# Performance work log

Hardware: AMD Instinct MI355X
Metric: run time of the kernel (lower is better)

## Reference

```python
import jax, jax.numpy as jnp
import numpy as np

N = 50000   # num_nodes
E = 640000  # num_edges (avg degree ~12.8)
D = 128     # input_dim
H = 128     # hidden_dim
T = 100     # targets per head


def setup_inputs() -> dict:
    key = jax.random.key(0)
    ks = jax.random.split(key, 20)
    w = lambda k, s: jax.random.normal(k, s, jnp.float32) * 0.02
    return {
        "x": jax.random.normal(ks[0], (N, D), jnp.float32),
        "edge_index": jax.random.randint(ks[1], (2, E), 0, N, dtype=jnp.int32),
        "edge_weight": jax.random.uniform(ks[2], (E,), jnp.float32),
        "ace_idx": jax.random.randint(ks[3], (T,), 0, N, dtype=jnp.int32),
        "h2_idx": jax.random.randint(ks[4], (T,), 0, N, dtype=jnp.int32),
        "W1": w(ks[5], (D, H)), "b1": jnp.zeros((H,), jnp.float32),
        "W2": w(ks[6], (H, H)), "b2": jnp.zeros((H,), jnp.float32),
        "W3": w(ks[7], (H, H)), "b3": jnp.zeros((H,), jnp.float32),
        "Wh": w(ks[8], (H, H)), "bh": jnp.zeros((H,), jnp.float32),
        "Wace": w(ks[9], (H, 1)), "bace": jnp.zeros((1,), jnp.float32),
        "Wh2": w(ks[10], (H, 1)), "bh2": jnp.zeros((1,), jnp.float32),
    }


def gcn_conv(x, src, dst, ew, W, b):
    # PyG GCNConv: add self-loops (weight 1), symmetric D^-1/2 (A+I) D^-1/2, then XW + b
    n = x.shape[0]
    xw = x @ W                                             # [N, H]
    deg = jax.ops.segment_sum(ew, dst, num_segments=n) + 1.0  # +1 from self-loop
    dinv = jax.lax.rsqrt(jnp.maximum(deg, 1e-12))          # deg >= 1 here
    norm = dinv[src] * ew * dinv[dst]                      # per-edge coefficient
    agg = jax.ops.segment_sum(norm[:, None] * xw[src], dst, num_segments=n)
    agg = agg + (dinv * dinv)[:, None] * xw                # self-loop contribution
    return agg + b


def reference(x, edge_index, edge_weight, ace_idx, h2_idx,
              W1, b1, W2, b2, W3, b3, Wh, bh, Wace, bace, Wh2, bh2):
    src, dst = edge_index[0], edge_index[1]
    h = jax.nn.relu(gcn_conv(x, src, dst, edge_weight, W1, b1))
    h = jax.nn.relu(gcn_conv(h, src, dst, edge_weight, W2, b2))
    h = jax.nn.relu(gcn_conv(h, src, dst, edge_weight, W3, b3))
    # dropout is identity in eval mode
    h = jax.nn.relu(h @ Wh + bh)
    ace_pred = h[ace_idx] @ Wace + bace   # [T, 1]
    h2_pred = h[h2_idx] @ Wh2 + bh2       # [T, 1]
    return jnp.concatenate([ace_pred, h2_pred], axis=0)  # [2T, 1]
```

## Files before the change

### kernel.cpp

```cpp
#include <hip/hip_runtime.h>
#include <math.h>

constexpr int N = 50000;
constexpr int E = 640000;
constexpr int D = 128;
constexpr int T = 100;
constexpr int MAXDEG = 64;
constexpr float SC = 256.0f;
constexpr float SCINV = 1.0f / 256.0f;
constexpr int GB = (N + 127) / 128;
constexpr int ESL = E / 4;
constexpr int EB4 = ESL / 256;
constexpr int ZB = N * 8 / 16 / 256 + 1;
constexpr int WCB = 3 * 16384 / 256;

typedef __attribute__((ext_vector_type(8))) _Float16 half8v;
typedef __attribute__((ext_vector_type(8))) unsigned short ushort8v;
typedef __attribute__((ext_vector_type(4))) float f32x4;

__device__ inline float dinv_of(unsigned int degY) {
  return 1.0f / sqrtf((float)degY * (1.0f / 16777216.0f) + 1.0f);
}


__global__ __launch_bounds__(256) void init_kernel(
    const float* __restrict__ W1, const float* __restrict__ W2,
    const float* __restrict__ W3, uint4* __restrict__ degcnt_v,
    unsigned short* __restrict__ wt0, unsigned short* __restrict__ wt1,
    unsigned short* __restrict__ w3kn) {
  int b = blockIdx.x, tid = threadIdx.x;
  if (b < ZB) {
    int i = b * 256 + tid;
    if (i < N * 8 / 16) degcnt_v[i] = uint4{0, 0, 0, 0};
  } else {
    int idx = (b - ZB) * 256 + tid;
    int layer = idx >> 14;
    int r = idx & 16383;
    if (layer == 0) {
      int n = r >> 7, k = r & 127;
      _Float16 h = (_Float16)(W1[k * D + n] * SC);
      wt0[n * D + k] = *(unsigned short*)&h;
    } else if (layer == 1) {
      int n = r >> 7, k = r & 127;
      _Float16 h = (_Float16)W2[k * D + n];
      wt1[n * D + k] = *(unsigned short*)&h;
    } else {
      int k = r >> 7, n = r & 127;
      _Float16 h = (_Float16)W3[k * D + n];
      w3kn[k * D + n] = *(unsigned short*)&h;
    }
  }
}


__global__ __launch_bounds__(256) void fused_eg1_kernel(
    const float* __restrict__ ew, const int* __restrict__ src,
    const int* __restrict__ dst,
    unsigned long long* __restrict__ degcnt, unsigned int* __restrict__ slot,
    const float* __restrict__ x, const unsigned short* __restrict__ Bt,
    unsigned short* __restrict__ z1) {
  const int b = blockIdx.x;
  const int tid = threadIdx.x;
  if (b < EB4) {
    int gid = b * 256 + tid;
    float w0 = ew[gid + 0 * ESL], w1 = ew[gid + 1 * ESL];
    float w2 = ew[gid + 2 * ESL], w3 = ew[gid + 3 * ESL];
    int d0 = dst[gid + 0 * ESL], d1 = dst[gid + 1 * ESL];
    int d2 = dst[gid + 2 * ESL], d3 = dst[gid + 3 * ESL];
    int s0 = src[gid + 0 * ESL], s1 = src[gid + 1 * ESL];
    int s2 = src[gid + 2 * ESL], s3 = src[gid + 3 * ESL];
#pragma unroll
    for (int j = 0; j < 4; ++j) {
      float w = j == 0 ? w0 : j == 1 ? w1 : j == 2 ? w2 : w3;
      int d   = j == 0 ? d0 : j == 1 ? d1 : j == 2 ? d2 : d3;
      int s   = j == 0 ? s0 : j == 1 ? s1 : j == 2 ? s2 : s3;
      unsigned int fxdeg = __float2uint_rn(w * 16777216.0f);
      unsigned int fx16 = __float2uint_rn(w * 65536.0f);
      if (fx16 > 65535u) fx16 = 65535u;
      unsigned long long old = atomicAdd(&degcnt[d],
                                         ((unsigned long long)fxdeg << 32) | 1ull);
      unsigned int rank = (unsigned int)(old & 0xffffffffull);
      if (rank < MAXDEG)
        slot[(size_t)d * MAXDEG + rank] = (fx16 << 16) | (unsigned int)s;
    }
  } else {
    const int w = tid >> 6, lane = tid & 63;
    const int q = lane >> 4, n16 = lane & 15;
    const int rbase = w * 32;
    const int row0 = (b - EB4) * 128;
    size_t arow[2];
#pragma unroll
    for (int rt = 0; rt < 2; ++rt) {
      int gr = row0 + rbase + rt * 16 + n16;
      if (gr >= N) gr = N - 1;
      arow[rt] = (size_t)gr * D;
    }
    half8v a[4][2];
#pragma unroll
    for (int kc = 0; kc < 4; ++kc) {
      const int ko = kc * 32 + q * 8;
#pragma unroll
      for (int rt = 0; rt < 2; ++rt) {
        float4 v0 = *(const float4*)&x[arow[rt] + ko];
        float4 v1 = *(const float4*)&x[arow[rt] + ko + 4];
        half8v h;
        h[0] = (_Float16)v0.x; h[1] = (_Float16)v0.y;
        h[2] = (_Float16)v0.z; h[3] = (_Float16)v0.w;
        h[4] = (_Float16)v1.x; h[5] = (_Float16)v1.y;
        h[6] = (_Float16)v1.z; h[7] = (_Float16)v1.w;
        a[kc][rt] = h;
      }
    }
    f32x4 acc[2][8] = {};
#pragma unroll
    for (int kc = 0; kc < 4; ++kc) {
      const int ko = kc * 32 + q * 8;
#pragma unroll
      for (int ct = 0; ct < 8; ++ct) {
        int n = ct * 16 + n16;
        half8v bb = *(const half8v*)&Bt[n * D + ko];
#pragma unroll
        for (int rt = 0; rt < 2; ++rt) {
          acc[rt][ct] = __builtin_amdgcn_mfma_f32_16x16x32_f16(a[kc][rt], bb, acc[rt][ct], 0, 0, 0);
        }
      }
    }
#pragma unroll
    for (int rt = 0; rt < 2; ++rt) {
#pragma unroll
      for (int r = 0; r < 4; ++r) {
        int gr = row0 + rbase + rt * 16 + q * 4 + r;
        if (gr < N) {
#pragma unroll
          for (int ct = 0; ct < 8; ++ct) {
            int col = ct * 16 + n16;
            _Float16 h = (_Float16)acc[rt][ct][r];
            z1[(size_t)gr * D + col] = *(unsigned short*)&h;
          }
        }
      }
    }
  }
}


__global__ __launch_bounds__(256) void gemm2_kernel(
    const unsigned short* __restrict__ A, const unsigned short* __restrict__ Bt,
    const uint2* __restrict__ degcnt, unsigned short* __restrict__ out) {
  const int tid = threadIdx.x;
  const int w = tid >> 6, lane = tid & 63;
  const int q = lane >> 4, n16 = lane & 15;
  const int rbase = w * 32;
  const int row0 = blockIdx.x * 128;

  size_t arow[2];
#pragma unroll
  for (int rt = 0; rt < 2; ++rt) {
    int gr = row0 + rbase + rt * 16 + n16;
    if (gr >= N) gr = N - 1;
    arow[rt] = (size_t)gr * D;
  }
  half8v a[4][2];
#pragma unroll
  for (int kc = 0; kc < 4; ++kc) {
    const int ko = kc * 32 + q * 8;
#pragma unroll
    for (int rt = 0; rt < 2; ++rt)
      a[kc][rt] = *(const half8v*)&A[arow[rt] + ko];
  }
  f32x4 acc[2][8] = {};
#pragma unroll
  for (int kc = 0; kc < 4; ++kc) {
    const int ko = kc * 32 + q * 8;
#pragma unroll
    for (int ct = 0; ct < 8; ++ct) {
      int n = ct * 16 + n16;
      half8v b = *(const half8v*)&Bt[n * D + ko];
#pragma unroll
      for (int rt = 0; rt < 2; ++rt) {
        acc[rt][ct] = __builtin_amdgcn_mfma_f32_16x16x32_f16(a[kc][rt], b, acc[rt][ct], 0, 0, 0);
      }
    }
  }
#pragma unroll
  for (int rt = 0; rt < 2; ++rt) {
#pragma unroll
    for (int r = 0; r < 4; ++r) {
      int gr = row0 + rbase + rt * 16 + q * 4 + r;
      if (gr < N) {
        float dv = dinv_of(degcnt[gr].y);
#pragma unroll
        for (int ct = 0; ct < 8; ++ct) {
          int col = ct * 16 + n16;
          _Float16 h = (_Float16)(acc[rt][ct][r] * dv);
          out[(size_t)gr * D + col] = *(unsigned short*)&h;
        }
      }
    }
  }
}


__global__ __launch_bounds__(256) void agg_kernel(
    const unsigned short* __restrict__ z, const unsigned int* __restrict__ slot,
    const uint2* __restrict__ degcnt, const float* __restrict__ bias,
    unsigned short* __restrict__ oP) {
  int g = (blockIdx.x * 256 + threadIdx.x) >> 4;
  int lane = threadIdx.x & 15;
  const unsigned int* degY = (const unsigned int*)degcnt;

  uint2 pg = degcnt[g];
  int cnt = (int)pg.x; if (cnt > MAXDEG) cnt = MAXDEG;
  float dvg = dinv_of(pg.y);
  half8v xv = *(const half8v*)&z[(size_t)g * D + lane * 8];
  float acc[8];
#pragma unroll
  for (int i = 0; i < 8; ++i) acc[i] = dvg * (float)xv[i];

  const unsigned int* sl = slot + (size_t)g * MAXDEG;
  int k = 0;
  for (; k + 4 <= cnt; k += 4) {
    uint4 p = *(const uint4*)&sl[k];
    float d0 = dinv_of(degY[((p.x & 0xffffu) << 1) + 1]);
    float d1 = dinv_of(degY[((p.y & 0xffffu) << 1) + 1]);
    float d2 = dinv_of(degY[((p.z & 0xffffu) << 1) + 1]);
    float d3 = dinv_of(degY[((p.w & 0xffffu) << 1) + 1]);
    float c0 = (float)(p.x >> 16) * (1.0f / 65536.0f) * d0;
    float c1 = (float)(p.y >> 16) * (1.0f / 65536.0f) * d1;
    float c2 = (float)(p.z >> 16) * (1.0f / 65536.0f) * d2;
    float c3 = (float)(p.w >> 16) * (1.0f / 65536.0f) * d3;
    half8v v0 = *(const half8v*)&z[(size_t)(p.x & 0xffffu) * D + lane * 8];
    half8v v1 = *(const half8v*)&z[(size_t)(p.y & 0xffffu) * D + lane * 8];
    half8v v2 = *(const half8v*)&z[(size_t)(p.z & 0xffffu) * D + lane * 8];
    half8v v3 = *(const half8v*)&z[(size_t)(p.w & 0xffffu) * D + lane * 8];
#pragma unroll
    for (int i = 0; i < 8; ++i) {
      acc[i] = fmaf(c0, (float)v0[i], acc[i]);
      acc[i] = fmaf(c1, (float)v1[i], acc[i]);
      acc[i] = fmaf(c2, (float)v2[i], acc[i]);
      acc[i] = fmaf(c3, (float)v3[i], acc[i]);
    }
  }
  for (; k < cnt; ++k) {
    unsigned int p = sl[k];
    float dsv = dinv_of(degY[((p & 0xffffu) << 1) + 1]);
    float c = (float)(p >> 16) * (1.0f / 65536.0f) * dsv;
    half8v v = *(const half8v*)&z[(size_t)(p & 0xffffu) * D + lane * 8];
#pragma unroll
    for (int i = 0; i < 8; ++i) acc[i] = fmaf(c, (float)v[i], acc[i]);
  }

  half8v hv;
#pragma unroll
  for (int i = 0; i < 8; ++i)
    hv[i] = (_Float16)fmaxf(fmaf(dvg, acc[i], bias[lane * 8 + i] * SC), 0.f);
  *(half8v*)&oP[(size_t)g * D + lane * 8] = hv;
}


__global__ __launch_bounds__(256) void l23_part_kernel(
    const unsigned short* __restrict__ z2, const unsigned int* __restrict__ slot,
    const uint2* __restrict__ degcnt, const float* __restrict__ b2,
    const int* __restrict__ ace_idx, const int* __restrict__ h2_idx,
    float* __restrict__ pacc) {
  __shared__ float sacc[16][128];
  int b = blockIdx.x;
  int t = b >> 2, p = b & 3;
  int tid = threadIdx.x;
  int node = (t < T) ? ace_idx[t] : h2_idx[t - T];

  int grp = tid >> 4, lane = tid & 15;
  int G = p * 16 + grp;
  float b2l[8];
#pragma unroll
  for (int i = 0; i < 8; ++i) b2l[i] = b2[lane * 8 + i] * SC;

  uint2 pn = degcnt[node];
  int tcnt = (int)pn.x; if (tcnt > MAXDEG) tcnt = MAXDEG;
  const unsigned int* tsl = slot + (size_t)node * MAXDEG;
  int nitems = 1 + tcnt;
  float a[8] = {};
  for (int it = G; it < nitems; it += 64) {
    int u; float wgt;
    if (it == 0) { u = node; wgt = 1.0f; }
    else {
      unsigned int pk = tsl[it - 1];
      wgt = (float)(pk >> 16) * (1.0f / 65536.0f);
      u = (int)(pk & 0xffffu);
    }
    uint2 pu = degcnt[u];
    float dvu = dinv_of(pu.y);
    int cu = (int)pu.x; if (cu > MAXDEG) cu = MAXDEG;
    half8v xv = *(const half8v*)&z2[(size_t)u * D + lane * 8];
    float r[8];
#pragma unroll
    for (int i = 0; i < 8; ++i) r[i] = (float)xv[i];
    const unsigned int* usl = slot + (size_t)u * MAXDEG;
    int e = 0;
    for (; e + 4 <= cu; e += 4) {
      uint4 p4 = *(const uint4*)&usl[e];
      float c0 = (float)(p4.x >> 16) * (1.0f / 65536.0f);
      float c1 = (float)(p4.y >> 16) * (1.0f / 65536.0f);
      float c2 = (float)(p4.z >> 16) * (1.0f / 65536.0f);
      float c3 = (float)(p4.w >> 16) * (1.0f / 65536.0f);
      half8v v0 = *(const half8v*)&z2[(size_t)(p4.x & 0xffffu) * D + lane * 8];
      half8v v1 = *(const half8v*)&z2[(size_t)(p4.y & 0xffffu) * D + lane * 8];
      half8v v2 = *(const half8v*)&z2[(size_t)(p4.z & 0xffffu) * D + lane * 8];
      half8v v3 = *(const half8v*)&z2[(size_t)(p4.w & 0xffffu) * D + lane * 8];
#pragma unroll
      for (int i = 0; i < 8; ++i) {
        r[i] = fmaf(c0, (float)v0[i], r[i]);
        r[i] = fmaf(c1, (float)v1[i], r[i]);
        r[i] = fmaf(c2, (float)v2[i], r[i]);
        r[i] = fmaf(c3, (float)v3[i], r[i]);
      }
    }
    for (; e < cu; ++e) {
      unsigned int p2 = usl[e];
      float c2 = (float)(p2 >> 16) * (1.0f / 65536.0f);
      half8v v = *(const half8v*)&z2[(size_t)(p2 & 0xffffu) * D + lane * 8];
#pragma unroll
      for (int i = 0; i < 8; ++i) r[i] = fmaf(c2, (float)v[i], r[i]);
    }
#pragma unroll
    for (int i = 0; i < 8; ++i) {
      float h2 = fmaxf(fmaf(dvu, r[i], b2l[i]), 0.f);
      a[i] = fmaf(wgt, dvu * h2, a[i]);
    }
  }
#pragma unroll
  for (int i = 0; i < 8; ++i) sacc[grp][lane * 8 + i] = a[i];
  __syncthreads();

  if (tid < 128) {
    float s = 0.f;
#pragma unroll
    for (int gp = 0; gp < 16; ++gp) s += sacc[gp][tid];
    pacc[(size_t)(t * 4 + p) * 128 + tid] = s;
  }
}


__global__ __launch_bounds__(256) void l23_finish_kernel(
    const uint2* __restrict__ degcnt, const float* __restrict__ pacc,
    const float* __restrict__ b3, const unsigned short* __restrict__ w3kn,
    const float* __restrict__ Wh, const float* __restrict__ bh,
    const int* __restrict__ ace_idx, const int* __restrict__ h2_idx,
    const float* __restrict__ Wace, const float* __restrict__ bace,
    const float* __restrict__ Wh2, const float* __restrict__ bh2,
    float* __restrict__ out) {
  __shared__ unsigned short w3l[16384];
  __shared__ float svec[128];
  __shared__ float h3v[128];
  __shared__ float psum[2];
  int t = blockIdx.x;
  int tid = threadIdx.x;
  int node; const float* whead; float bhead;
  if (t < T) { node = ace_idx[t];     whead = Wace; bhead = bace[0]; }
  else       { node = h2_idx[t - T];  whead = Wh2;  bhead = bh2[0]; }

#pragma unroll
  for (int it = 0; it < 8; ++it) {
    int idx = tid + it * 256;
    *(ushort8v*)&w3l[idx * 8] = *(const ushort8v*)&w3kn[idx * 8];
  }
  if (tid < 128) {
    const float* pa = &pacc[(size_t)t * 4 * 128];
    float s = pa[tid] + pa[128 + tid] + pa[256 + tid] + pa[384 + tid];
    svec[tid] = s * dinv_of(degcnt[node].y);
  }
  __syncthreads();

  if (tid < 128) {
    float y = b3[tid] * SC;
#pragma unroll 16
    for (int k = 0; k < 128; ++k) {
      _Float16 wv = *(const _Float16*)&w3l[k * D + tid];
      y = fmaf(svec[k], (float)wv, y);
    }
    h3v[tid] = fmaxf(y, 0.f) * SCINV;
  }
  __syncthreads();

  float v = 0.f;
  if (tid < 128) {
    float acc = bh[tid];
#pragma unroll 16
    for (int k = 0; k < 128; ++k)
      acc = fmaf(h3v[k], Wh[k * D + tid], acc);
    v = fmaxf(acc, 0.f) * whead[tid];
  }
#pragma unroll
  for (int off = 32; off; off >>= 1) v += __shfl_down(v, off, 64);
  if (tid < 128 && (tid & 63) == 0) psum[tid >> 6] = v;
  __syncthreads();
  if (tid == 0) out[t] = psum[0] + psum[1] + bhead;
}


extern "C" void kernel_launch(void* const* d_in, const int* in_sizes, int n_in,
                              void* d_out, int out_size, void* d_ws, size_t ws_size,
                              hipStream_t stream) {
  const float* x    = (const float*)d_in[0];
  const int*   ei   = (const int*)d_in[1];
  const float* ew   = (const float*)d_in[2];
  const int*   ace  = (const int*)d_in[3];
  const int*   h2   = (const int*)d_in[4];
  const float* W1 = (const float*)d_in[5];  const float* b1 = (const float*)d_in[6];
  const float* W2 = (const float*)d_in[7];  const float* b2 = (const float*)d_in[8];
  const float* W3 = (const float*)d_in[9];  const float* b3 = (const float*)d_in[10];
  const float* Wh = (const float*)d_in[11]; const float* bh = (const float*)d_in[12];
  const float* Wace = (const float*)d_in[13]; const float* bace = (const float*)d_in[14];
  const float* Wh2  = (const float*)d_in[15]; const float* bh2  = (const float*)d_in[16];
  const int* src = ei;
  const int* dst = ei + E;

  char* w = (char*)d_ws;
  unsigned long long* degcnt = (unsigned long long*)w;  w += (size_t)N * 8;
  unsigned int* slot = (unsigned int*)w;  w += (size_t)N * MAXDEG * 4;
  unsigned short* wt0 = (unsigned short*)w;  w += 16384 * 2;
  unsigned short* wt1 = (unsigned short*)w;  w += 16384 * 2;
  unsigned short* w3kn = (unsigned short*)w; w += 16384 * 2;
  float* pacc = (float*)w;                   w += (size_t)2 * T * 4 * 128 * 4;
  unsigned short* zbuf = (unsigned short*)w; w += (size_t)N * D * 2;
  unsigned short* P1  = (unsigned short*)w;  w += (size_t)N * D * 2;

  const int AG = N * 16 / 256;

  init_kernel<<<ZB + WCB, 256, 0, stream>>>(W1, W2, W3, (uint4*)degcnt, wt0, wt1, w3kn);
  fused_eg1_kernel<<<EB4 + GB, 256, 0, stream>>>(ew, src, dst, degcnt, slot, x, wt0, zbuf);
  agg_kernel<<<AG, 256, 0, stream>>>(zbuf, slot, (const uint2*)degcnt, b1, P1);
  gemm2_kernel<<<GB, 256, 0, stream>>>(P1, wt1, (const uint2*)degcnt, zbuf);
  l23_part_kernel<<<4 * 2 * T, 256, 0, stream>>>(zbuf, slot, (const uint2*)degcnt,
                                                 b2, ace, h2, pacc);
  l23_finish_kernel<<<2 * T, 256, 0, stream>>>((const uint2*)degcnt, pacc, b3, w3kn,
                                               Wh, bh, ace, h2,
                                               Wace, bace, Wh2, bh2, (float*)d_out);
}
```

Before: 212.4 us.

## Reorder fused GEMM/edge kernel blocks, one edge per thread, unroll gathers by 8

```diff
diff --git a/kernel.cpp b/kernel.cpp
--- a/kernel.cpp
+++ b/kernel.cpp
@@ -9,9 +9,9 @@
 constexpr float SC = 256.0f;
 constexpr float SCINV = 1.0f / 256.0f;
 constexpr int GB = (N + 127) / 128;
-constexpr int ESL = E / 4;
-constexpr int EB4 = ESL / 256;
-constexpr int ZB = N * 8 / 16 / 256 + 1;
+constexpr int EBLK = (E + 255) / 256;
+constexpr int ZTOT = N * 8 / 16;
+constexpr int ZB = (ZTOT + 255) / 256;
 constexpr int WCB = 3 * 16384 / 256;
 
 typedef __attribute__((ext_vector_type(8))) _Float16 half8v;
@@ -25,13 +25,13 @@
 
 __global__ __launch_bounds__(256) void init_kernel(
     const float* __restrict__ W1, const float* __restrict__ W2,
-    const float* __restrict__ W3, uint4* __restrict__ degcnt_v,
+    const float* __restrict__ W3, uint4* __restrict__ zero_v,
     unsigned short* __restrict__ wt0, unsigned short* __restrict__ wt1,
     unsigned short* __restrict__ w3kn) {
   int b = blockIdx.x, tid = threadIdx.x;
   if (b < ZB) {
     int i = b * 256 + tid;
-    if (i < N * 8 / 16) degcnt_v[i] = uint4{0, 0, 0, 0};
+    if (i < ZTOT) zero_v[i] = uint4{0, 0, 0, 0};
   } else {
     int idx = (b - ZB) * 256 + tid;
     int layer = idx >> 14;
@@ -53,27 +53,19 @@
 }
 
 
-__global__ __launch_bounds__(256) void fused_eg1_kernel(
+__global__ __launch_bounds__(256) void fused_g1e_kernel(
+    const float* __restrict__ x, const unsigned short* __restrict__ Bt,
+    unsigned short* __restrict__ z1,
     const float* __restrict__ ew, const int* __restrict__ src,
     const int* __restrict__ dst,
-    unsigned long long* __restrict__ degcnt, unsigned int* __restrict__ slot,
-    const float* __restrict__ x, const unsigned short* __restrict__ Bt,
-    unsigned short* __restrict__ z1) {
+    unsigned long long* __restrict__ degcnt, unsigned int* __restrict__ slot) {
   const int b = blockIdx.x;
   const int tid = threadIdx.x;
-  if (b < EB4) {
-    int gid = b * 256 + tid;
-    float w0 = ew[gid + 0 * ESL], w1 = ew[gid + 1 * ESL];
-    float w2 = ew[gid + 2 * ESL], w3 = ew[gid + 3 * ESL];
-    int d0 = dst[gid + 0 * ESL], d1 = dst[gid + 1 * ESL];
-    int d2 = dst[gid + 2 * ESL], d3 = dst[gid + 3 * ESL];
-    int s0 = src[gid + 0 * ESL], s1 = src[gid + 1 * ESL];
-    int s2 = src[gid + 2 * ESL], s3 = src[gid + 3 * ESL];
-#pragma unroll
-    for (int j = 0; j < 4; ++j) {
-      float w = j == 0 ? w0 : j == 1 ? w1 : j == 2 ? w2 : w3;
-      int d   = j == 0 ? d0 : j == 1 ? d1 : j == 2 ? d2 : d3;
-      int s   = j == 0 ? s0 : j == 1 ? s1 : j == 2 ? s2 : s3;
+  if (b >= GB) {
+    int e = (b - GB) * 256 + tid;
+    if (e < E) {
+      float w = ew[e];
+      int d = dst[e];
       unsigned int fxdeg = __float2uint_rn(w * 16777216.0f);
       unsigned int fx16 = __float2uint_rn(w * 65536.0f);
       if (fx16 > 65535u) fx16 = 65535u;
@@ -81,62 +73,62 @@
                                          ((unsigned long long)fxdeg << 32) | 1ull);
       unsigned int rank = (unsigned int)(old & 0xffffffffull);
       if (rank < MAXDEG)
-        slot[(size_t)d * MAXDEG + rank] = (fx16 << 16) | (unsigned int)s;
-    }
-  } else {
-    const int w = tid >> 6, lane = tid & 63;
-    const int q = lane >> 4, n16 = lane & 15;
-    const int rbase = w * 32;
-    const int row0 = (b - EB4) * 128;
-    size_t arow[2];
+        slot[(size_t)d * MAXDEG + rank] = (fx16 << 16) | (unsigned int)src[e];
+    }
+    return;
+  }
+  const int w = tid >> 6, lane = tid & 63;
+  const int q = lane >> 4, n16 = lane & 15;
+  const int rbase = w * 32;
+  const int row0 = b * 128;
+  size_t arow[2];
+#pragma unroll
+  for (int rt = 0; rt < 2; ++rt) {
+    int gr = row0 + rbase + rt * 16 + n16;
+    if (gr >= N) gr = N - 1;
+    arow[rt] = (size_t)gr * D;
+  }
+  half8v a[4][2];
+#pragma unroll
+  for (int kc = 0; kc < 4; ++kc) {
+    const int ko = kc * 32 + q * 8;
 #pragma unroll
     for (int rt = 0; rt < 2; ++rt) {
-      int gr = row0 + rbase + rt * 16 + n16;
-      if (gr >= N) gr = N - 1;
-      arow[rt] = (size_t)gr * D;
-    }
-    half8v a[4][2];
-#pragma unroll
-    for (int kc = 0; kc < 4; ++kc) {
-      const int ko = kc * 32 + q * 8;
+      float4 v0 = *(const float4*)&x[arow[rt] + ko];
+      float4 v1 = *(const float4*)&x[arow[rt] + ko + 4];
+      half8v h;
+      h[0] = (_Float16)v0.x; h[1] = (_Float16)v0.y;
+      h[2] = (_Float16)v0.z; h[3] = (_Float16)v0.w;
+      h[4] = (_Float16)v1.x; h[5] = (_Float16)v1.y;
+      h[6] = (_Float16)v1.z; h[7] = (_Float16)v1.w;
+      a[kc][rt] = h;
+    }
+  }
+  f32x4 acc[2][8] = {};
+#pragma unroll
+  for (int kc = 0; kc < 4; ++kc) {
+    const int ko = kc * 32 + q * 8;
+#pragma unroll
+    for (int ct = 0; ct < 8; ++ct) {
+      int n = ct * 16 + n16;
+      half8v bb = *(const half8v*)&Bt[n * D + ko];
 #pragma unroll
       for (int rt = 0; rt < 2; ++rt) {
-        float4 v0 = *(const float4*)&x[arow[rt] + ko];
-        float4 v1 = *(const float4*)&x[arow[rt] + ko + 4];
-        half8v h;
-        h[0] = (_Float16)v0.x; h[1] = (_Float16)v0.y;
-        h[2] = (_Float16)v0.z; h[3] = (_Float16)v0.w;
-        h[4] = (_Float16)v1.x; h[5] = (_Float16)v1.y;
-        h[6] = (_Float16)v1.z; h[7] = (_Float16)v1.w;
-        a[kc][rt] = h;
-      }
-    }
-    f32x4 acc[2][8] = {};
-#pragma unroll
-    for (int kc = 0; kc < 4; ++kc) {
-      const int ko = kc * 32 + q * 8;
-#pragma unroll
-      for (int ct = 0; ct < 8; ++ct) {
-        int n = ct * 16 + n16;
-        half8v bb = *(const half8v*)&Bt[n * D + ko];
-#pragma unroll
-        for (int rt = 0; rt < 2; ++rt) {
-          acc[rt][ct] = __builtin_amdgcn_mfma_f32_16x16x32_f16(a[kc][rt], bb, acc[rt][ct], 0, 0, 0);
-        }
-      }
-    }
-#pragma unroll
-    for (int rt = 0; rt < 2; ++rt) {
-#pragma unroll
-      for (int r = 0; r < 4; ++r) {
-        int gr = row0 + rbase + rt * 16 + q * 4 + r;
-        if (gr < N) {
-#pragma unroll
-          for (int ct = 0; ct < 8; ++ct) {
-            int col = ct * 16 + n16;
-            _Float16 h = (_Float16)acc[rt][ct][r];
-            z1[(size_t)gr * D + col] = *(unsigned short*)&h;
-          }
+        acc[rt][ct] = __builtin_amdgcn_mfma_f32_16x16x32_f16(a[kc][rt], bb, acc[rt][ct], 0, 0, 0);
+      }
+    }
+  }
+#pragma unroll
+  for (int rt = 0; rt < 2; ++rt) {
+#pragma unroll
+    for (int r = 0; r < 4; ++r) {
+      int gr = row0 + rbase + rt * 16 + q * 4 + r;
+      if (gr < N) {
+#pragma unroll
+        for (int ct = 0; ct < 8; ++ct) {
+          int col = ct * 16 + n16;
+          _Float16 h = (_Float16)acc[rt][ct][r];
+          z1[(size_t)gr * D + col] = *(unsigned short*)&h;
         }
       }
     }
@@ -219,16 +211,47 @@
 
   const unsigned int* sl = slot + (size_t)g * MAXDEG;
   int k = 0;
+  for (; k + 8 <= cnt; k += 8) {
+    uint4 pA = *(const uint4*)&sl[k];
+    uint4 pB = *(const uint4*)&sl[k + 4];
+    unsigned int s0 = pA.x & 0xffffu, s1 = pA.y & 0xffffu;
+    unsigned int s2 = pA.z & 0xffffu, s3 = pA.w & 0xffffu;
+    unsigned int s4 = pB.x & 0xffffu, s5 = pB.y & 0xffffu;
+    unsigned int s6 = pB.z & 0xffffu, s7 = pB.w & 0xffffu;
+    float c0 = (float)(pA.x >> 16) * (1.0f / 65536.0f) * dinv_of(degY[(s0 << 1) + 1]);
+    float c1 = (float)(pA.y >> 16) * (1.0f / 65536.0f) * dinv_of(degY[(s1 << 1) + 1]);
+    float c2 = (float)(pA.z >> 16) * (1.0f / 65536.0f) * dinv_of(degY[(s2 << 1) + 1]);
+    float c3 = (float)(pA.w >> 16) * (1.0f / 65536.0f) * dinv_of(degY[(s3 << 1) + 1]);
+    float c4 = (float)(pB.x >> 16) * (1.0f / 65536.0f) * dinv_of(degY[(s4 << 1) + 1]);
+    float c5 = (float)(pB.y >> 16) * (1.0f / 65536.0f) * dinv_of(degY[(s5 << 1) + 1]);
+    float c6 = (float)(pB.z >> 16) * (1.0f / 65536.0f) * dinv_of(degY[(s6 << 1) + 1]);
+    float c7 = (float)(pB.w >> 16) * (1.0f / 65536.0f) * dinv_of(degY[(s7 << 1) + 1]);
+    half8v v0 = *(const half8v*)&z[(size_t)s0 * D + lane * 8];
+    half8v v1 = *(const half8v*)&z[(size_t)s1 * D + lane * 8];
+    half8v v2 = *(const half8v*)&z[(size_t)s2 * D + lane * 8];
+    half8v v3 = *(const half8v*)&z[(size_t)s3 * D + lane * 8];
+    half8v v4 = *(const half8v*)&z[(size_t)s4 * D + lane * 8];
+    half8v v5 = *(const half8v*)&z[(size_t)s5 * D + lane * 8];
+    half8v v6 = *(const half8v*)&z[(size_t)s6 * D + lane * 8];
+    half8v v7 = *(const half8v*)&z[(size_t)s7 * D + lane * 8];
+#pragma unroll
+    for (int i = 0; i < 8; ++i) {
+      acc[i] = fmaf(c0, (float)v0[i], acc[i]);
+      acc[i] = fmaf(c1, (float)v1[i], acc[i]);
+      acc[i] = fmaf(c2, (float)v2[i], acc[i]);
+      acc[i] = fmaf(c3, (float)v3[i], acc[i]);
+      acc[i] = fmaf(c4, (float)v4[i], acc[i]);
+      acc[i] = fmaf(c5, (float)v5[i], acc[i]);
+      acc[i] = fmaf(c6, (float)v6[i], acc[i]);
+      acc[i] = fmaf(c7, (float)v7[i], acc[i]);
+    }
+  }
   for (; k + 4 <= cnt; k += 4) {
     uint4 p = *(const uint4*)&sl[k];
-    float d0 = dinv_of(degY[((p.x & 0xffffu) << 1) + 1]);
-    float d1 = dinv_of(degY[((p.y & 0xffffu) << 1) + 1]);
-    float d2 = dinv_of(degY[((p.z & 0xffffu) << 1) + 1]);
-    float d3 = dinv_of(degY[((p.w & 0xffffu) << 1) + 1]);
-    float c0 = (float)(p.x >> 16) * (1.0f / 65536.0f) * d0;
-    float c1 = (float)(p.y >> 16) * (1.0f / 65536.0f) * d1;
-    float c2 = (float)(p.z >> 16) * (1.0f / 65536.0f) * d2;
-    float c3 = (float)(p.w >> 16) * (1.0f / 65536.0f) * d3;
+    float c0 = (float)(p.x >> 16) * (1.0f / 65536.0f) * dinv_of(degY[(((p.x & 0xffffu)) << 1) + 1]);
+    float c1 = (float)(p.y >> 16) * (1.0f / 65536.0f) * dinv_of(degY[(((p.y & 0xffffu)) << 1) + 1]);
+    float c2 = (float)(p.z >> 16) * (1.0f / 65536.0f) * dinv_of(degY[(((p.z & 0xffffu)) << 1) + 1]);
+    float c3 = (float)(p.w >> 16) * (1.0f / 65536.0f) * dinv_of(degY[(((p.w & 0xffffu)) << 1) + 1]);
     half8v v0 = *(const half8v*)&z[(size_t)(p.x & 0xffffu) * D + lane * 8];
     half8v v1 = *(const half8v*)&z[(size_t)(p.y & 0xffffu) * D + lane * 8];
     half8v v2 = *(const half8v*)&z[(size_t)(p.z & 0xffffu) * D + lane * 8];
@@ -297,6 +320,37 @@
     for (int i = 0; i < 8; ++i) r[i] = (float)xv[i];
     const unsigned int* usl = slot + (size_t)u * MAXDEG;
     int e = 0;
+    for (; e + 8 <= cu; e += 8) {
+      uint4 pA = *(const uint4*)&usl[e];
+      uint4 pB = *(const uint4*)&usl[e + 4];
+      float c0 = (float)(pA.x >> 16) * (1.0f / 65536.0f);
+      float c1 = (float)(pA.y >> 16) * (1.0f / 65536.0f);
+      float c2 = (float)(pA.z >> 16) * (1.0f / 65536.0f);
+      float c3 = (float)(pA.w >> 16) * (1.0f / 65536.0f);
+      float c4 = (float)(pB.x >> 16) * (1.0f / 65536.0f);
+      float c5 = (float)(pB.y >> 16) * (1.0f / 65536.0f);
+      float c6 = (float)(pB.z >> 16) * (1.0f / 65536.0f);
+      float c7 = (float)(pB.w >> 16) * (1.0f / 65536.0f);
+      half8v v0 = *(const half8v*)&z2[(size_t)(pA.x & 0xffffu) * D + lane * 8];
+      half8v v1 = *(const half8v*)&z2[(size_t)(pA.y & 0xffffu) * D + lane * 8];
+      half8v v2 = *(const half8v*)&z2[(size_t)(pA.z & 0xffffu) * D + lane * 8];
+      half8v v3 = *(const half8v*)&z2[(size_t)(pA.w & 0xffffu) * D + lane * 8];
+      half8v v4 = *(const half8v*)&z2[(size_t)(pB.x & 0xffffu) * D + lane * 8];
+      half8v v5 = *(const half8v*)&z2[(size_t)(pB.y & 0xffffu) * D + lane * 8];
+      half8v v6 = *(const half8v*)&z2[(size_t)(pB.z & 0xffffu) * D + lane * 8];
+      half8v v7 = *(const half8v*)&z2[(size_t)(pB.w & 0xffffu) * D + lane * 8];
+#pragma unroll
+      for (int i = 0; i < 8; ++i) {
+        r[i] = fmaf(c0, (float)v0[i], r[i]);
+        r[i] = fmaf(c1, (float)v1[i], r[i]);
+        r[i] = fmaf(c2, (float)v2[i], r[i]);
+        r[i] = fmaf(c3, (float)v3[i], r[i]);
+        r[i] = fmaf(c4, (float)v4[i], r[i]);
+        r[i] = fmaf(c5, (float)v5[i], r[i]);
+        r[i] = fmaf(c6, (float)v6[i], r[i]);
+        r[i] = fmaf(c7, (float)v7[i], r[i]);
+      }
+    }
     for (; e + 4 <= cu; e += 4) {
       uint4 p4 = *(const uint4*)&usl[e];
       float c0 = (float)(p4.x >> 16) * (1.0f / 65536.0f);
@@ -417,7 +471,7 @@
 
   char* w = (char*)d_ws;
   unsigned long long* degcnt = (unsigned long long*)w;  w += (size_t)N * 8;
-  unsigned int* slot = (unsigned int*)w;  w += (size_t)N * MAXDEG * 4;
+  unsigned int* slot = (unsigned int*)w;     w += (size_t)N * MAXDEG * 4;
   unsigned short* wt0 = (unsigned short*)w;  w += 16384 * 2;
   unsigned short* wt1 = (unsigned short*)w;  w += 16384 * 2;
   unsigned short* w3kn = (unsigned short*)w; w += 16384 * 2;
@@ -428,7 +482,7 @@
   const int AG = N * 16 / 256;
 
   init_kernel<<<ZB + WCB, 256, 0, stream>>>(W1, W2, W3, (uint4*)degcnt, wt0, wt1, w3kn);
-  fused_eg1_kernel<<<EB4 + GB, 256, 0, stream>>>(ew, src, dst, degcnt, slot, x, wt0, zbuf);
+  fused_g1e_kernel<<<GB + EBLK, 256, 0, stream>>>(x, wt0, zbuf, ew, src, dst, degcnt, slot);
   agg_kernel<<<AG, 256, 0, stream>>>(zbuf, slot, (const uint2*)degcnt, b1, P1);
   gemm2_kernel<<<GB, 256, 0, stream>>>(P1, wt1, (const uint2*)degcnt, zbuf);
   l23_part_kernel<<<4 * 2 * T, 256, 0, stream>>>(zbuf, slot, (const uint2*)degcnt,
```

Result: no change. 210.9 us (-0.7%).
